# Optimization experiments

Measured on AMD Instinct MI355X. Metric: run time of the kernel, lower is better.

## Reference

```python
import jax, jax.numpy as jnp
import numpy as np

BN_EPS = 1e-5

def setup_inputs() -> dict:
    key = jax.random.key(0)
    ks = jax.random.split(key, 10)
    B, C, W, H = 4, 128, 32, 128
    Co = C // 2  # 64
    s_in = 1.0 / np.sqrt(C)
    s_out = 1.0 / np.sqrt(Co)
    return {
        "range_x": jax.random.normal(ks[0], (B, C, W, H), jnp.float32),
        "img": jax.random.normal(ks[1], (B, C, W, H), jnp.float32),
        "wq": jax.random.normal(ks[2], (Co, C), jnp.float32) * s_in,
        "bq": jax.random.normal(ks[3], (Co,), jnp.float32) * 0.01,
        "wk": jax.random.normal(ks[4], (Co, C), jnp.float32) * s_in,
        "bk": jax.random.normal(ks[5], (Co,), jnp.float32) * 0.01,
        "wv": jax.random.normal(ks[6], (Co, C), jnp.float32) * s_in,
        "bv": jax.random.normal(ks[7], (Co,), jnp.float32) * 0.01,
        "wc": jax.random.normal(ks[8], (C, Co), jnp.float32) * s_out,
        "bc": jax.random.normal(ks[9], (C,), jnp.float32) * 0.01,
        "bn_gamma": jnp.ones((C,), jnp.float32),
        "bn_beta": jnp.zeros((C,), jnp.float32),
        "bn_mean": jnp.zeros((C,), jnp.float32),
        "bn_var": jnp.ones((C,), jnp.float32),
    }

def reference(range_x, img, wq, bq, wk, bk, wv, bv, wc, bc, bn_gamma, bn_beta, bn_mean, bn_var):
    B, C, W, H = range_x.shape
    HW = W * H
    r = range_x.reshape(B, C, HW)  # [B,C,N]
    i = img.reshape(B, C, HW)
    # 1x1 convs == per-pixel linear projections
    q = jnp.einsum('oc,bcn->bno', wq, r) + bq            # [B,N,Co] (query from range)
    k = jnp.einsum('oc,bcn->bon', wk, i) + bk[None, :, None]  # [B,Co,N]
    corr = jnp.einsum('bno,bom->bnm', q, k)              # [B,N,N]
    attn = jax.nn.softmax(corr, axis=-1)
    v = jnp.einsum('oc,bcn->bon', wv, i) + bv[None, :, None]  # [B,Co,N]
    # out[b,o,n] = sum_m v[b,o,m] * attn[b,n,m]  (bmm(V, attn^T))
    out = jnp.einsum('bom,bnm->bon', v, attn)            # [B,Co,N]
    # channel_back: 1x1 conv -> BN (inference) -> ReLU
    y = jnp.einsum('co,bon->bcn', wc, out) + bc[None, :, None]
    inv = bn_gamma / jnp.sqrt(bn_var + BN_EPS)
    y = y * inv[None, :, None] + (bn_beta - bn_mean * inv)[None, :, None]
    y = jax.nn.relu(y)
    return img + y.reshape(B, C, W, H)
```

## Files before the change

kernel.cpp:

```cpp
#include <hip/hip_runtime.h>
#include <hip/hip_bf16.h>

typedef __attribute__((ext_vector_type(4))) float f32x4;
typedef __attribute__((ext_vector_type(8))) short s16x8;
typedef __attribute__((ext_vector_type(4))) short s16x4;

#define LOG2E 1.4426950408889634f

__device__ __forceinline__ ushort f2bf(float f){
  union { float f; unsigned u; } x; x.f = f;
  unsigned r = x.u + 0x7fffu + ((x.u >> 16) & 1u);
  return (ushort)(r >> 16);
}
__device__ __forceinline__ float bf2f(ushort h){
  union { unsigned u; float f; } x; x.u = ((unsigned)h) << 16;
  return x.f;
}

__device__ __forceinline__ float fexp2(float x){
#if __has_builtin(__builtin_amdgcn_exp2f)
  return __builtin_amdgcn_exp2f(x);
#else
  float r; asm("v_exp_f32 %0, %1" : "=v"(r) : "v"(x)); return r;
#endif
}

__device__ __forceinline__ void gload16(const void* g, void* l){
  __builtin_amdgcn_global_load_lds(
      (const __attribute__((address_space(1))) void*)g,
      (__attribute__((address_space(3))) void*)l, 16, 0, 0);
}

#if __has_builtin(__builtin_amdgcn_mfma_f32_16x16x16bf16_1k)
__device__ __forceinline__ f32x4 mfma16(s16x4 a, s16x4 b, f32x4 c){
  return __builtin_amdgcn_mfma_f32_16x16x16bf16_1k(a, b, c, 0, 0, 0);
}
#elif __has_builtin(__builtin_amdgcn_mfma_f32_16x16x16_bf16)
__device__ __forceinline__ f32x4 mfma16(s16x4 a, s16x4 b, f32x4 c){
  return __builtin_amdgcn_mfma_f32_16x16x16_bf16(a, b, c, 0, 0, 0);
}
#else
__device__ __forceinline__ f32x4 mfma16(s16x4 a, s16x4 b, f32x4 c){
  f32x4 d;
  asm volatile("v_mfma_f32_16x16x16_bf16 %0, %1, %2, %3\n\ts_nop 7\n\ts_nop 7"
               : "=v"(d) : "v"(a), "v"(b), "v"(c));
  return d;
}
#endif

__global__ __launch_bounds__(256, 4) void proj_qkv(
    const float* __restrict__ xr, const float* __restrict__ xi,
    const float* __restrict__ wq, const float* __restrict__ wk,
    const float* __restrict__ wv,
    const float* __restrict__ bq, const float* __restrict__ bk,
    const float* __restrict__ bv,
    ushort* __restrict__ Qh, ushort* __restrict__ Ql,
    ushort* __restrict__ Kh, ushort* __restrict__ Vt)
{
  __shared__ __align__(16) float xL[128*64];
  const int tid = threadIdx.x;
  const int idx = blockIdx.x;
  const int oq  = idx & 3;
  const int nt  = (idx >> 2) & 63;
  const int b   = idx >> 8;
  const int n0  = nt << 6;
  const int lane = tid & 63;
  const int w    = tid >> 6;
  const int l15  = lane & 15;
  const int g    = lane >> 4;
  const int obase = oq << 4;

  #define STAGE_X(src)                                                    \
  {                                                                       \
    const float* xs = (src) + (size_t)b*524288 + n0;                      \
    _Pragma("unroll")                                                     \
    for (int j = 0; j < 8; ++j){                                          \
      int row = j*16 + (tid >> 4);                                        \
      int ch  = tid & 15;                                                 \
      gload16(xs + (size_t)row*4096 + ch*4, xL + j*1024 + w*256);         \
    }                                                                     \
  }
  #define BUILD_FRAGS(fh, fl)                                             \
  {                                                                       \
    const int px = w*16 + l15;                                            \
    _Pragma("unroll")                                                     \
    for (int kc = 0; kc < 4; ++kc){                                       \
      _Pragma("unroll")                                                   \
      for (int j = 0; j < 8; ++j){                                        \
        int r = kc*32 + g*8 + j;                                          \
        float a = xL[r*64 + px];                                          \
        ushort h = f2bf(a);                                               \
        fh[kc][j] = (short)h;                                             \
        fl[kc][j] = (short)f2bf(a - bf2f(h));                             \
      }                                                                   \
    }                                                                     \
  }
  #define LOAD_WFRAGS(wp, wh, wl4)                                        \
  {                                                                       \
    _Pragma("unroll")                                                     \
    for (int kc = 0; kc < 4; ++kc){                                       \
      const float* src = (wp) + (obase + l15)*128 + kc*32 + g*8;          \
      f32x4 a0 = *(const f32x4*)(src);                                    \
      f32x4 a1 = *(const f32x4*)(src + 4);                                \
      _Pragma("unroll")                                                   \
      for (int e = 0; e < 4; ++e){                                        \
        ushort h0 = f2bf(a0[e]);                                          \
        wh[kc][e]   = (short)h0;                                          \
        wl4[kc][e]  = (short)f2bf(a0[e] - bf2f(h0));                      \
        ushort h1 = f2bf(a1[e]);                                          \
        wh[kc][4+e]  = (short)h1;                                         \
        wl4[kc][4+e] = (short)f2bf(a1[e] - bf2f(h1));                     \
      }                                                                   \
    }                                                                     \
  }

  STAGE_X(xr);
  __syncthreads();
  {
    s16x8 xh[4], xl4[4];
    BUILD_FRAGS(xh, xl4);
    s16x8 wfh[4], wfl[4];
    LOAD_WFRAGS(wq, wfh, wfl);
    f32x4 acc = {0.f,0.f,0.f,0.f};
    #pragma unroll
    for (int kc = 0; kc < 4; ++kc){
      acc = __builtin_amdgcn_mfma_f32_16x16x32_bf16(xh[kc],  wfh[kc], acc, 0,0,0);
      acc = __builtin_amdgcn_mfma_f32_16x16x32_bf16(xl4[kc], wfh[kc], acc, 0,0,0);
      acc = __builtin_amdgcn_mfma_f32_16x16x32_bf16(xh[kc],  wfl[kc], acc, 0,0,0);
    }
    float bqv = bq[obase + l15];
    #pragma unroll
    for (int r = 0; r < 4; ++r){
      float q = (acc[r] + bqv) * LOG2E;
      ushort hi = f2bf(q);
      size_t a = (size_t)(b*4096 + n0 + w*16 + g*4 + r)*64 + obase + l15;
      Qh[a] = hi; Ql[a] = f2bf(q - bf2f(hi));
    }
  }
  __syncthreads();

  STAGE_X(xi);
  __syncthreads();
  {
    s16x8 xh[4], xl4[4];
    BUILD_FRAGS(xh, xl4);
    {
      s16x8 wfh[4], wfl[4];
      LOAD_WFRAGS(wk, wfh, wfl);
      f32x4 acc = {0.f,0.f,0.f,0.f};
      #pragma unroll
      for (int kc = 0; kc < 4; ++kc){
        acc = __builtin_amdgcn_mfma_f32_16x16x32_bf16(xh[kc],  wfh[kc], acc, 0,0,0);
        acc = __builtin_amdgcn_mfma_f32_16x16x32_bf16(xl4[kc], wfh[kc], acc, 0,0,0);
        acc = __builtin_amdgcn_mfma_f32_16x16x32_bf16(xh[kc],  wfl[kc], acc, 0,0,0);
      }
      float bkv = bk[obase + l15];
      #pragma unroll
      for (int r = 0; r < 4; ++r){
        size_t a = (size_t)(b*4096 + n0 + w*16 + g*4 + r)*64 + obase + l15;
        Kh[a] = f2bf(acc[r] + bkv);
      }
    }
    {
      s16x8 wfh[4], wfl[4];
      LOAD_WFRAGS(wv, wfh, wfl);
      f32x4 acc = {0.f,0.f,0.f,0.f};
      #pragma unroll
      for (int kc = 0; kc < 4; ++kc){
        acc = __builtin_amdgcn_mfma_f32_16x16x32_bf16(wfh[kc], xh[kc],  acc, 0,0,0);
        acc = __builtin_amdgcn_mfma_f32_16x16x32_bf16(wfl[kc], xh[kc],  acc, 0,0,0);
        acc = __builtin_amdgcn_mfma_f32_16x16x32_bf16(wfh[kc], xl4[kc], acc, 0,0,0);
      }
      #pragma unroll
      for (int r = 0; r < 4; ++r){
        int o = obase + g*4 + r;
        float v = acc[r] + bv[o];
        Vt[(size_t)(b*64 + o)*4096 + n0 + w*16 + l15] = f2bf(v);
      }
    }
  }
  #undef STAGE_X
  #undef BUILD_FRAGS
  #undef LOAD_WFRAGS
}

__global__ __launch_bounds__(256, 5) void flash_attn(
    const ushort* __restrict__ Qh, const ushort* __restrict__ Ql,
    const ushort* __restrict__ Kh, const ushort* __restrict__ Vt,
    float* __restrict__ Opart, float* __restrict__ Mst,
    float* __restrict__ Lst)
{
  __shared__ __align__(16) ushort khL[2][4096];
  __shared__ __align__(16) ushort vL[2][4096];

  const int tid  = threadIdx.x;
  const int idx  = blockIdx.x;
  const int xcd  = idx & 7;
  const int rest = idx >> 3;
  const int b    = xcd >> 1;
  const int ks   = ((xcd & 1) << 1) | (rest >> 6);
  const int qt   = rest & 63;
  const int lane = tid & 63;
  const int w    = tid >> 6;
  const int l15  = lane & 15;
  const int g    = lane >> 4;
  const int qrow = qt*64 + w*16;
  const int kv0  = ks << 10;
  const int srow = lane >> 2;
  const int sg   = lane & 3;
  const int sgs  = sg ^ ((srow >> 1) & 3);

  const size_t qoff = ((size_t)(b*4096 + qrow + l15))*64 + g*8;
  s16x8 qh0 = *(const s16x8*)(Qh + qoff);
  s16x8 qh1 = *(const s16x8*)(Qh + qoff + 32);
  s16x8 ql0 = *(const s16x8*)(Ql + qoff);
  s16x8 ql1 = *(const s16x8*)(Ql + qoff + 32);

  const char* KhB = (const char*)(Kh + (size_t)b*4096*64);
  const char* VB  = (const char*)(Vt + (size_t)b*64*4096);

  f32x4 o_acc[4];
  #pragma unroll
  for (int ot=0;ot<4;++ot) o_acc[ot] = (f32x4){0.f,0.f,0.f,0.f};
  float m_run = -1e30f, l_run = 0.f;

  #define STAGE_KV(kvb, bi)                                               \
  {                                                                       \
    size_t kr = (size_t)((kvb) + w*16 + srow)*128 + sgs*16;               \
    char* kd = (char*)khL[bi] + w*2048;                                   \
    gload16(KhB + kr,      kd);                                           \
    gload16(KhB + kr + 64, kd + 1024);                                    \
    size_t vr = (size_t)(w*16 + srow)*8192 + (size_t)(kvb)*2 + sgs*16;    \
    char* vd = (char*)vL[bi] + w*2048;                                    \
    gload16(VB + vr,      vd);                                            \
    gload16(VB + vr + 64, vd + 1024);                                     \
  }

  STAGE_KV(kv0, 0);
  __syncthreads();

  const int swz = (l15 >> 1) & 3;
  const int kfrag = l15*64 + (g ^ swz)*16;

  for (int t = 0; t < 16; ++t){
    const int cb = t & 1;

    if (t < 15){
      STAGE_KV(kv0 + (t+1)*64, cb ^ 1);
    }

    f32x4 s[4];
    #pragma unroll
    for (int ct=0; ct<4; ++ct){
      const char* kb = (const char*)khL[cb] + ct*2048;
      s16x8 kh0 = *(const s16x8*)(kb + kfrag);
      s16x8 kh1 = *(const s16x8*)(kb + 1024 + kfrag);
      f32x4 acc = {0.f,0.f,0.f,0.f};
      acc = __builtin_amdgcn_mfma_f32_16x16x32_bf16(kh0, ql0, acc, 0, 0, 0);
      acc = __builtin_amdgcn_mfma_f32_16x16x32_bf16(kh1, ql1, acc, 0, 0, 0);
      acc = __builtin_amdgcn_mfma_f32_16x16x32_bf16(kh0, qh0, acc, 0, 0, 0);
      acc = __builtin_amdgcn_mfma_f32_16x16x32_bf16(kh1, qh1, acc, 0, 0, 0);
      s[ct] = acc;
    }

    float mx = s[0][0];
    #pragma unroll
    for (int ct=0;ct<4;++ct){
      #pragma unroll
      for (int r=0;r<4;++r) mx = fmaxf(mx, s[ct][r]);
    }
    mx = fmaxf(mx, __shfl_xor(mx, 16));
    mx = fmaxf(mx, __shfl_xor(mx, 32));
    if (!__all(mx <= m_run + 8.0f)){
      float mn = fmaxf(m_run, mx);
      float sc = fexp2(m_run - mn);
      m_run = mn;
      l_run *= sc;
      #pragma unroll
      for (int ot=0;ot<4;++ot) o_acc[ot] *= sc;
    }
    float rs = 0.f;
    s16x4 pbf[4];
    #pragma unroll
    for (int ct=0;ct<4;++ct){
      #pragma unroll
      for (int r=0;r<4;++r){
        float p = fexp2(s[ct][r] - m_run);
        rs += p;
        pbf[ct][r] = (short)f2bf(p);
      }
    }
    rs += __shfl_xor(rs, 16);
    rs += __shfl_xor(rs, 32);
    l_run += rs;

    #pragma unroll
    for (int ot=0; ot<4; ++ot){
      const char* vbase = (const char*)vL[cb] + ot*2048 + l15*64;
      #pragma unroll
      for (int ct=0; ct<4; ++ct){
        int chunk = (((ct & 1) << 1) + (g >> 1)) ^ swz;
        s16x4 av = *(const s16x4*)(vbase + (ct>>1)*1024 + chunk*16 + (g&1)*8);
        o_acc[ot] = mfma16(av, pbf[ct], o_acc[ot]);
      }
    }

    __syncthreads();
  }
  #undef STAGE_KV

  float* ep = (float*)((char*)vL + (size_t)w*4096);
  #pragma unroll
  for (int ot=0;ot<4;++ot){
    int dw = l15*64 + ((ot*16 + g*4) ^ ((l15 & 7) << 2));
    *(f32x4*)(ep + dw) = o_acc[ot];
  }
  __syncthreads();
  {
    const int q4  = lane >> 2;
    const int seg = lane & 3;
    float* Ob = Opart + ((size_t)(ks*4 + b)*4096 + qrow)*64;
    #pragma unroll
    for (int c=0;c<4;++c){
      int o0 = seg*16 + c*4;
      f32x4 vv = *(const f32x4*)(ep + q4*64 + (o0 ^ ((q4 & 7) << 2)));
      *(f32x4*)(Ob + (size_t)q4*64 + o0) = vv;
    }
  }
  if (lane < 16){
    Mst[(size_t)(ks*4 + b)*4096 + qrow + lane] = m_run;
    Lst[(size_t)(ks*4 + b)*4096 + qrow + lane] = l_run;
  }
}

__global__ __launch_bounds__(256) void final_proj(
    const float* __restrict__ Opart, const float* __restrict__ Mst,
    const float* __restrict__ Lst, const float* __restrict__ wc,
    const float* __restrict__ bc, const float* __restrict__ gm,
    const float* __restrict__ bt, const float* __restrict__ mu,
    const float* __restrict__ vr, const float* __restrict__ img,
    float* __restrict__ out)
{
  __shared__ float ol[64*64];
  __shared__ float scl[4][64];
  const int tid = threadIdx.x;
  const int idx = blockIdx.x;
  const int cs  = idx & 1;
  const int nt  = (idx >> 1) & 63;
  const int b   = idx >> 7;
  const int n0  = nt << 6;

  if (tid < 64){
    size_t rid = (size_t)b*4096 + n0 + tid;
    float m0 = Mst[0*16384 + rid], m1 = Mst[1*16384 + rid];
    float m2 = Mst[2*16384 + rid], m3 = Mst[3*16384 + rid];
    float mm = fmaxf(fmaxf(m0,m1), fmaxf(m2,m3));
    float s0 = fexp2(m0-mm), s1 = fexp2(m1-mm);
    float s2 = fexp2(m2-mm), s3 = fexp2(m3-mm);
    float li = s0*Lst[0*16384+rid] + s1*Lst[1*16384+rid]
             + s2*Lst[2*16384+rid] + s3*Lst[3*16384+rid];
    float inv = 1.0f / li;
    scl[0][tid] = s0*inv; scl[1][tid] = s1*inv;
    scl[2][tid] = s2*inv; scl[3][tid] = s3*inv;
  }
  __syncthreads();

  {
    const size_t base = ((size_t)b*4096 + n0)*64;
    for (int j=0;j<16;++j){
      int flat = tid + (j << 8);
      int n = flat >> 6, o = flat & 63;
      float v = Opart[0*(size_t)16384*64 + base + flat] * scl[0][n]
              + Opart[1*(size_t)16384*64 + base + flat] * scl[1][n]
              + Opart[2*(size_t)16384*64 + base + flat] * scl[2][n]
              + Opart[3*(size_t)16384*64 + base + flat] * scl[3][n];
      ol[(o << 6) + (n ^ (o & 31))] = v;
    }
  }
  __syncthreads();

  const int lane = tid & 63;
  const int w = __builtin_amdgcn_readfirstlane(tid >> 6);
  const int c0 = (cs << 6) + (w << 4);

  float acc[16];
  #pragma unroll
  for (int cc=0;cc<16;++cc) acc[cc] = 0.f;

  for (int o=0;o<64;++o){
    float v = ol[(o << 6) + (lane ^ (o & 31))];
    #pragma unroll
    for (int cc=0;cc<16;++cc)
      acc[cc] = fmaf(wc[(c0+cc)*64 + o], v, acc[cc]);
  }

  #pragma unroll
  for (int cc=0;cc<16;++cc){
    int c = c0 + cc;
    float inv = gm[c] * rsqrtf(vr[c] + 1e-5f);
    float sh  = bt[c] - mu[c]*inv;
    float y = (acc[cc] + bc[c]) * inv + sh;
    y = fmaxf(y, 0.f);
    size_t gi = ((size_t)(b*128 + c))*4096 + n0 + lane;
    out[gi] = img[gi] + y;
  }
}

extern "C" void kernel_launch(void* const* d_in, const int* in_sizes, int n_in,
                              void* d_out, int out_size, void* d_ws, size_t ws_size,
                              hipStream_t stream)
{
  const float* xr = (const float*)d_in[0];
  const float* xi = (const float*)d_in[1];
  const float* wq = (const float*)d_in[2];
  const float* bq = (const float*)d_in[3];
  const float* wk = (const float*)d_in[4];
  const float* bk = (const float*)d_in[5];
  const float* wv = (const float*)d_in[6];
  const float* bv = (const float*)d_in[7];
  const float* wc = (const float*)d_in[8];
  const float* bc = (const float*)d_in[9];
  const float* gm = (const float*)d_in[10];
  const float* bt = (const float*)d_in[11];
  const float* mu = (const float*)d_in[12];
  const float* vr = (const float*)d_in[13];
  float* out = (float*)d_out;

  const size_t SZ = (size_t)4*4096*64;
  ushort* Qhw = (ushort*)d_ws;
  ushort* Qlw = Qhw + SZ;
  ushort* Khw = Qlw + SZ;
  ushort* Vtw = Khw + SZ;
  float*  Ow  = (float*)(Vtw + SZ);
  float*  Mw  = Ow + (size_t)16*4096*64;
  float*  Lw  = Mw + (size_t)16*4096;

  proj_qkv  <<<1024, 256, 0, stream>>>(xr, xi, wq, wk, wv, bq, bk, bv,
                                       Qhw, Qlw, Khw, Vtw);
  flash_attn<<<1024, 256, 0, stream>>>(Qhw, Qlw, Khw, Vtw, Ow, Mw, Lw);
  final_proj<<<512,  256, 0, stream>>>(Ow, Mw, Lw, wc, bc, gm, bt, mu, vr, xi, out);
}
```

Baseline: 83.65 us.

## Retile QKV projection so each block owns 16 pixels across all output channels

The projection kernel used to stage 64 pixels × 128 channels of input per block, with each block computing only a 16-channel slice of the outputs, so every pixel tile was loaded four times by different blocks. Now each block stages 16 pixels × 128 channels and its four waves cover all 64 output channels. This removes the redundant global reads of the input and shrinks shared memory from 32KB to 8KB, which allows more resident blocks. In exchange each block does less work per launch, and each 16-byte chunk covers only 16 contiguous pixels, so global loads are less coalesced.

```diff
diff --git a/kernel.cpp b/kernel.cpp
--- a/kernel.cpp
+++ b/kernel.cpp
@@ -57,38 +57,36 @@
     ushort* __restrict__ Qh, ushort* __restrict__ Ql,
     ushort* __restrict__ Kh, ushort* __restrict__ Vt)
 {
-  __shared__ __align__(16) float xL[128*64];
+  __shared__ __align__(16) float xL[128*16];
   const int tid = threadIdx.x;
   const int idx = blockIdx.x;
-  const int oq  = idx & 3;
-  const int nt  = (idx >> 2) & 63;
+  const int nt  = idx & 255;
   const int b   = idx >> 8;
-  const int n0  = nt << 6;
+  const int n0  = nt << 4;
   const int lane = tid & 63;
   const int w    = tid >> 6;
   const int l15  = lane & 15;
   const int g    = lane >> 4;
-  const int obase = oq << 4;
-
-  #define STAGE_X(src)                                                    \
+  const int obase = w << 4;
+
+  #define STAGE_X16(src)                                                  \
   {                                                                       \
     const float* xs = (src) + (size_t)b*524288 + n0;                      \
     _Pragma("unroll")                                                     \
-    for (int j = 0; j < 8; ++j){                                          \
-      int row = j*16 + (tid >> 4);                                        \
-      int ch  = tid & 15;                                                 \
-      gload16(xs + (size_t)row*4096 + ch*4, xL + j*1024 + w*256);         \
+    for (int rdd = 0; rdd < 2; ++rdd){                                    \
+      int chunk = rdd*256 + tid;                              \
+      int c = chunk >> 2, p4 = chunk & 3;                                 \
+      gload16(xs + (size_t)c*4096 + p4*4, xL + rdd*1024 + w*256);         \
     }                                                                     \
   }
-  #define BUILD_FRAGS(fh, fl)                                             \
+  #define BUILD_FRAGS16(fh, fl)                                           \
   {                                                                       \
-    const int px = w*16 + l15;                                            \
     _Pragma("unroll")                                                     \
     for (int kc = 0; kc < 4; ++kc){                                       \
       _Pragma("unroll")                                                   \
       for (int j = 0; j < 8; ++j){                                        \
-        int r = kc*32 + g*8 + j;                                          \
-        float a = xL[r*64 + px];                                          \
+        int c = kc*32 + g*8 + j;                                          \
+        float a = xL[c*16 + l15];                                         \
         ushort h = f2bf(a);                                               \
         fh[kc][j] = (short)h;                                             \
         fl[kc][j] = (short)f2bf(a - bf2f(h));                             \
@@ -114,11 +112,11 @@
     }                                                                     \
   }
 
-  STAGE_X(xr);
+  STAGE_X16(xr);
   __syncthreads();
   {
     s16x8 xh[4], xl4[4];
-    BUILD_FRAGS(xh, xl4);
+    BUILD_FRAGS16(xh, xl4);
     s16x8 wfh[4], wfl[4];
     LOAD_WFRAGS(wq, wfh, wfl);
     f32x4 acc = {0.f,0.f,0.f,0.f};
@@ -133,17 +131,17 @@
     for (int r = 0; r < 4; ++r){
       float q = (acc[r] + bqv) * LOG2E;
       ushort hi = f2bf(q);
-      size_t a = (size_t)(b*4096 + n0 + w*16 + g*4 + r)*64 + obase + l15;
+      size_t a = (size_t)(b*4096 + n0 + g*4 + r)*64 + obase + l15;
       Qh[a] = hi; Ql[a] = f2bf(q - bf2f(hi));
     }
   }
   __syncthreads();
 
-  STAGE_X(xi);
+  STAGE_X16(xi);
   __syncthreads();
   {
     s16x8 xh[4], xl4[4];
-    BUILD_FRAGS(xh, xl4);
+    BUILD_FRAGS16(xh, xl4);
     {
       s16x8 wfh[4], wfl[4];
       LOAD_WFRAGS(wk, wfh, wfl);
@@ -157,7 +155,7 @@
       float bkv = bk[obase + l15];
       #pragma unroll
       for (int r = 0; r < 4; ++r){
-        size_t a = (size_t)(b*4096 + n0 + w*16 + g*4 + r)*64 + obase + l15;
+        size_t a = (size_t)(b*4096 + n0 + g*4 + r)*64 + obase + l15;
         Kh[a] = f2bf(acc[r] + bkv);
       }
     }
@@ -175,12 +173,12 @@
       for (int r = 0; r < 4; ++r){
         int o = obase + g*4 + r;
         float v = acc[r] + bv[o];
-        Vt[(size_t)(b*64 + o)*4096 + n0 + w*16 + l15] = f2bf(v);
-      }
-    }
-  }
-  #undef STAGE_X
-  #undef BUILD_FRAGS
+        Vt[(size_t)(b*64 + o)*4096 + n0 + l15] = f2bf(v);
+      }
+    }
+  }
+  #undef STAGE_X16
+  #undef BUILD_FRAGS16
   #undef LOAD_WFRAGS
 }
 
```

Measured after the change: 81.07 us. 1.03x faster.
